# Kernel tuning notes

Measured on AMD Instinct MI355X. Metric: run time of the kernel, lower is better.

## Reference

```python
import jax, jax.numpy as jnp
import numpy as np

D_MODEL = 768
N_HEADS = 12
HEAD_DIM = D_MODEL // N_HEADS
BATCH = 1
SEQ = 4096


def setup_inputs() -> dict:
    key = jax.random.key(0)
    ks = jax.random.split(key, 5)
    std = 1.0 / np.sqrt(D_MODEL)
    return {
        "x": jax.random.normal(ks[0], (BATCH, SEQ, D_MODEL), dtype=jnp.float32),
        "Wq": jax.random.normal(ks[1], (D_MODEL, D_MODEL), dtype=jnp.float32) * std,
        "Wk": jax.random.normal(ks[2], (D_MODEL, D_MODEL), dtype=jnp.float32) * std,
        "Wv": jax.random.normal(ks[3], (D_MODEL, D_MODEL), dtype=jnp.float32) * std,
        "Wp": jax.random.normal(ks[4], (D_MODEL, D_MODEL), dtype=jnp.float32) * std,
    }


def reference(x, Wq, Wk, Wv, Wp):
    B, S, D = x.shape
    scale = HEAD_DIM ** -0.5
    # torch Linear: y = x @ W.T ; reshape to [B, H, S, hd]
    def split_heads(y):
        return y.reshape(B, S, N_HEADS, HEAD_DIM).transpose(0, 2, 1, 3)
    q = split_heads(x @ Wq.T)
    k = split_heads(x @ Wk.T)
    v = split_heads(x @ Wv.T)
    # full [B, H, S, S] scores, as in the original module
    att = jnp.einsum("bhqd,bhkd->bhqk", q, k) * scale
    causal = jnp.tril(jnp.ones((S, S), dtype=bool))
    att = jnp.where(causal[None, None], att, -jnp.inf)
    att = jax.nn.softmax(att, axis=-1)
    y = jnp.einsum("bhqk,bhkd->bhqd", att, v)
    y = y.transpose(0, 2, 1, 3).reshape(B, S, D)
    return y @ Wp.T
```

## Files before the change

kernel.cpp:

```cpp
#include <hip/hip_runtime.h>
#include <hip/hip_bf16.h>
#include <stdint.h>

#define DM 768
#define SQ 4096
#define NH 12

typedef __bf16 bf16;
typedef __bf16 bf16x8 __attribute__((ext_vector_type(8)));
typedef float floatx4 __attribute__((ext_vector_type(4)));
typedef short short4v __attribute__((ext_vector_type(4)));

#if defined(__has_builtin)
#if __has_builtin(__builtin_amdgcn_mfma_f32_16x16x16bf16_1k)
#define HAVE_MFMA16 1
#endif
#endif
#ifndef HAVE_MFMA16
#define HAVE_MFMA16 0
#endif

typedef __attribute__((address_space(1))) const uint32_t cu32_g;
typedef __attribute__((address_space(3))) uint32_t u32_l;

__device__ __forceinline__ uint16_t f2bf(float f) {
  uint32_t u = __builtin_bit_cast(uint32_t, f);
  u += 0x7fff + ((u >> 16) & 1);
  return (uint16_t)(u >> 16);
}

__device__ __forceinline__ uint32_t pk2(float lo, float hi) {
  __hip_bfloat162 h = __float22bfloat162_rn(float2{lo, hi});
  uint32_t u;
  __builtin_memcpy(&u, &h, 4);
  return u;
}

__device__ __forceinline__ float bflo(uint32_t u) {
  return __builtin_bit_cast(float, u << 16);
}
__device__ __forceinline__ float bfhi(uint32_t u) {
  return __builtin_bit_cast(float, u & 0xffff0000u);
}

__device__ __forceinline__ void async16(const bf16* g, bf16* l) {
  __builtin_amdgcn_global_load_lds((cu32_g*)g, (u32_l*)l, 16, 0, 0);
}

__global__ __launch_bounds__(256) void cvt_kernel(
    const float* __restrict__ x, const float* __restrict__ wq,
    const float* __restrict__ wk, const float* __restrict__ wv,
    const float* __restrict__ wp, bf16* __restrict__ xb, bf16* __restrict__ wqb,
    bf16* __restrict__ wkb, bf16* __restrict__ wvb, bf16* __restrict__ wpb) {
  const int XQ = (SQ * DM) / 4;
  const int WQ = (DM * DM) / 4;
  int t = blockIdx.x * 256 + threadIdx.x;
  const float* src;
  bf16* dst;
  int local;
  if (t < XQ) { src = x;  dst = xb;  local = t; }
  else if (t < XQ + WQ)     { src = wq; dst = wqb; local = t - XQ; }
  else if (t < XQ + 2 * WQ) { src = wk; dst = wkb; local = t - XQ - WQ; }
  else if (t < XQ + 3 * WQ) { src = wv; dst = wvb; local = t - XQ - 2 * WQ; }
  else                      { src = wp; dst = wpb; local = t - XQ - 3 * WQ; }
  float4 v = ((const float4*)src)[local];
  ushort4 o;
  o.x = f2bf(v.x); o.y = f2bf(v.y); o.z = f2bf(v.z); o.w = f2bf(v.w);
  ((ushort4*)dst)[local] = o;
}

__device__ __forceinline__ void gemm_core(const bf16* __restrict__ A,
                                          const bf16* __restrict__ B, int m0,
                                          int n0, floatx4 (&acc)[4][4]) {
  __shared__ bf16 lA[2 * 4096];
  __shared__ bf16 lB[2 * 4096];
  const int tid = threadIdx.x;
  const int lane = tid & 63;
  const int w = tid >> 6;

  const int r0 = w * 32 + (lane >> 2);
  const int ke = (((lane & 3) ^ ((lane >> 3) & 3))) * 8;
  const bf16* gA0 = A + (size_t)(m0 + r0) * DM + ke;
  const bf16* gA1 = A + (size_t)(m0 + r0 + 16) * DM + ke;
  const bf16* gB0 = B + (size_t)(n0 + r0) * DM + ke;
  const bf16* gB1 = B + (size_t)(n0 + r0 + 16) * DM + ke;

  async16(gA0, lA + w * 1024); async16(gA1, lA + w * 1024 + 512);
  async16(gB0, lB + w * 1024); async16(gB1, lB + w * 1024 + 512);
  gA0 += 32; gA1 += 32; gB0 += 32; gB1 += 32;

  const int mrow = (w >> 1) * 64 + (lane & 15);
  const int nrow = (w & 1) * 64 + (lane & 15);
  const int cswz = ((lane >> 4) ^ ((lane >> 1) & 3)) * 8;

  for (int kt = 0; kt < DM / 32; ++kt) {
    __syncthreads();
    if (kt + 1 < DM / 32) {
      const int nb = ((kt + 1) & 1) * 4096;
      async16(gA0, lA + nb + w * 1024); async16(gA1, lA + nb + w * 1024 + 512);
      async16(gB0, lB + nb + w * 1024); async16(gB1, lB + nb + w * 1024 + 512);
      gA0 += 32; gA1 += 32; gB0 += 32; gB1 += 32;
    }
    const int cb = (kt & 1) * 4096;
    bf16x8 a[4], b[4];
#pragma unroll
    for (int mt = 0; mt < 4; ++mt)
      a[mt] = *(const bf16x8*)&lA[cb + (mrow + mt * 16) * 32 + cswz];
#pragma unroll
    for (int nt = 0; nt < 4; ++nt)
      b[nt] = *(const bf16x8*)&lB[cb + (nrow + nt * 16) * 32 + cswz];
#pragma unroll
    for (int mt = 0; mt < 4; ++mt)
#pragma unroll
      for (int nt = 0; nt < 4; ++nt)
        acc[mt][nt] = __builtin_amdgcn_mfma_f32_16x16x32_bf16(
            a[mt], b[nt], acc[mt][nt], 0, 0, 0);
  }
}

__global__ __launch_bounds__(256) void qkv_kernel(
    const bf16* __restrict__ xb, const bf16* __restrict__ wq,
    const bf16* __restrict__ wk, const bf16* __restrict__ wv,
    bf16* __restrict__ Qb, bf16* __restrict__ Kb, bf16* __restrict__ Vtb) {
  const int z = blockIdx.z;
  const bf16* B = (z == 0) ? wq : (z == 1) ? wk : wv;
  const int m0 = blockIdx.x * 128, n0 = blockIdx.y * 128;
  floatx4 acc[4][4] = {};
  gemm_core(xb, B, m0, n0, acc);
  const int lane = threadIdx.x & 63, w = threadIdx.x >> 6;
  const int quad = lane >> 4, ql = lane & 15;
  const float qs = (z == 0) ? 0.18033688011112042f : 1.0f;
  if (z < 2) {
    bf16* C = (z == 0) ? Qb : Kb;
#pragma unroll
    for (int mt = 0; mt < 4; ++mt)
#pragma unroll
      for (int nt = 0; nt < 4; ++nt) {
        int row = m0 + (w >> 1) * 64 + mt * 16 + quad * 4;
        int col = n0 + (w & 1) * 64 + nt * 16 + ql;
#pragma unroll
        for (int r = 0; r < 4; ++r)
          *(uint16_t*)&C[(size_t)(row + r) * DM + col] = f2bf(acc[mt][nt][r] * qs);
      }
  } else {
#pragma unroll
    for (int mt = 0; mt < 4; ++mt)
#pragma unroll
      for (int nt = 0; nt < 4; ++nt) {
        int row = m0 + (w >> 1) * 64 + mt * 16 + quad * 4;
        int col = n0 + (w & 1) * 64 + nt * 16 + ql;
        uint32_t lo = pk2(acc[mt][nt][0], acc[mt][nt][1]);
        uint32_t hi = pk2(acc[mt][nt][2], acc[mt][nt][3]);
        *(uint2*)&Vtb[(size_t)col * SQ + row] = make_uint2(lo, hi);
      }
  }
}

__global__ __launch_bounds__(256) void proj_kernel(
    const bf16* __restrict__ Ob, const bf16* __restrict__ wp,
    float* __restrict__ out) {
  __shared__ bf16 lA[2 * 2048];
  __shared__ bf16 lB[2 * 4096];
  const int tid = threadIdx.x, lane = tid & 63, w = tid >> 6;
  const int m0 = blockIdx.x * 64, n0 = blockIdx.y * 128;

  const int ke = (((lane & 3) ^ ((lane >> 3) & 3))) * 8;
  const bf16* gA = Ob + (size_t)(m0 + w * 16 + (lane >> 2)) * DM + ke;
  const bf16* gB0 = wp + (size_t)(n0 + w * 32 + (lane >> 2)) * DM + ke;
  const bf16* gB1 = wp + (size_t)(n0 + w * 32 + (lane >> 2) + 16) * DM + ke;

  async16(gA, lA + w * 512);
  async16(gB0, lB + w * 1024); async16(gB1, lB + w * 1024 + 512);
  gA += 32; gB0 += 32; gB1 += 32;

  const int mrow = (w >> 1) * 32 + (lane & 15);
  const int nrow = (w & 1) * 64 + (lane & 15);
  const int cswz = ((lane >> 4) ^ ((lane >> 1) & 3)) * 8;
  floatx4 acc[2][4] = {};

  for (int kt = 0; kt < DM / 32; ++kt) {
    __syncthreads();
    if (kt + 1 < DM / 32) {
      const int nbA = ((kt + 1) & 1) * 2048, nbB = ((kt + 1) & 1) * 4096;
      async16(gA, lA + nbA + w * 512);
      async16(gB0, lB + nbB + w * 1024); async16(gB1, lB + nbB + w * 1024 + 512);
      gA += 32; gB0 += 32; gB1 += 32;
    }
    const int cbA = (kt & 1) * 2048, cbB = (kt & 1) * 4096;
    bf16x8 a[2], b[4];
#pragma unroll
    for (int mt = 0; mt < 2; ++mt)
      a[mt] = *(const bf16x8*)&lA[cbA + (mrow + mt * 16) * 32 + cswz];
#pragma unroll
    for (int nt = 0; nt < 4; ++nt)
      b[nt] = *(const bf16x8*)&lB[cbB + (nrow + nt * 16) * 32 + cswz];
#pragma unroll
    for (int mt = 0; mt < 2; ++mt)
#pragma unroll
      for (int nt = 0; nt < 4; ++nt)
        acc[mt][nt] = __builtin_amdgcn_mfma_f32_16x16x32_bf16(
            a[mt], b[nt], acc[mt][nt], 0, 0, 0);
  }
  const int quad = lane >> 4, ql = lane & 15;
#pragma unroll
  for (int mt = 0; mt < 2; ++mt)
#pragma unroll
    for (int nt = 0; nt < 4; ++nt) {
      int row = m0 + (w >> 1) * 32 + mt * 16 + quad * 4;
      int col = n0 + (w & 1) * 64 + nt * 16 + ql;
#pragma unroll
      for (int r = 0; r < 4; ++r)
        out[(size_t)(row + r) * DM + col] = acc[mt][nt][r];
    }
}

__global__ __launch_bounds__(256, 4) void attn_kernel(
    const bf16* __restrict__ Qb, const bf16* __restrict__ Kb,
    const bf16* __restrict__ Vtb, uint16_t* __restrict__ OpartB,
    float* __restrict__ Lpart, bf16* __restrict__ Ob) {
#if HAVE_MFMA16
  __shared__ __align__(16) char smem[32768];
#else
  __shared__ __align__(16) char smem[40960];
  bf16* lPt = (bf16*)(smem + 32768);
#endif
  const int tid = threadIdx.x, lane = tid & 63, w = tid >> 6;
  const int quad = lane >> 4, ql = lane & 15;

  int b = blockIdx.x;
  int h = b % NH;
  int i = b / NH;
  int qb, c;
  if (i < 32)      { qb = 31 - (i >> 2); c = i & 3; }
  else if (i < 56) { int t2 = i - 32; qb = 23 - t2 / 3; c = t2 % 3; }
  else if (i < 72) { int t2 = i - 56; qb = 15 - (t2 >> 1); c = t2 & 1; }
  else             { qb = 79 - i; c = 0; }
  const int kv0 = c * 1024;
  const int kv_end = min((qb + 1) * 128, kv0 + 1024);
  const int n_it = (kv_end - kv0) >> 6;
  const bool diag = (kv_end == (qb + 1) * 128);

  bf16x8 qf[2][2];
#pragma unroll
  for (int nt = 0; nt < 2; ++nt)
#pragma unroll
    for (int kt = 0; kt < 2; ++kt)
      qf[nt][kt] = *(const bf16x8*)&Qb[(size_t)(qb * 128 + w * 32 + nt * 16 + ql) * DM +
                                       h * 64 + kt * 32 + quad * 8];

  const int src_e = (((lane & 3) ^ ((lane >> 3) & 3))) * 8;
  const bf16* gK[2];
  const bf16* gV[2];
#pragma unroll
  for (int t = 0; t < 2; ++t) {
    int o = t * 4096 + w * 1024 + lane * 16;
    int cK = o >> 12, rK = (o & 4095) >> 6;
    gK[t] = Kb + (size_t)(kv0 + rK) * DM + h * 64 + cK * 32 + src_e;
    int dV = w * 16 + (lane >> 2);
    gV[t] = Vtb + (size_t)(h * 64 + dV) * SQ + kv0 + t * 32 + src_e;
  }

#pragma unroll
  for (int t = 0; t < 2; ++t) {
    async16(gK[t], (bf16*)(smem + t * 4096 + w * 1024));
    async16(gV[t], (bf16*)(smem + 8192 + t * 4096 + w * 1024));
    gK[t] += 64 * DM;
    gV[t] += 64;
  }

  floatx4 o_acc[4][2] = {};
  float l_s[2] = {0.f, 0.f};
  const int cswz = ((lane >> 4) ^ ((lane >> 1) & 3)) * 8;

  for (int j = 0; j < n_it; ++j) {
    __syncthreads();
    if (j + 1 < n_it) {
      char* dst = smem + ((j + 1) & 1) * 16384;
#pragma unroll
      for (int t = 0; t < 2; ++t) {
        async16(gK[t], (bf16*)(dst + t * 4096 + w * 1024));
        async16(gV[t], (bf16*)(dst + 8192 + t * 4096 + w * 1024));
        gK[t] += 64 * DM;
        gV[t] += 64;
      }
    }
    const char* cbuf = smem + (j & 1) * 16384;
    const bf16* kbuf = (const bf16*)cbuf;
    const char* vbuf = cbuf + 8192;

    floatx4 s[4][2] = {};
#pragma unroll
    for (int kt = 0; kt < 2; ++kt)
#pragma unroll
      for (int mt = 0; mt < 4; ++mt) {
        bf16x8 a = *(const bf16x8*)&kbuf[kt * 2048 + (mt * 16 + ql) * 32 + cswz];
#pragma unroll
        for (int nt = 0; nt < 2; ++nt)
          s[mt][nt] = __builtin_amdgcn_mfma_f32_16x16x32_bf16(a, qf[nt][kt],
                                                              s[mt][nt], 0, 0, 0);
      }

    if (diag && j + 2 >= n_it) {
      const int koff = (j + 1 == n_it) ? 64 : 0;
#pragma unroll
      for (int mt = 0; mt < 4; ++mt)
#pragma unroll
        for (int nt = 0; nt < 2; ++nt)
#pragma unroll
          for (int r = 0; r < 4; ++r) {
            int kpos = koff + mt * 16 + quad * 4 + r;
            int qpos = w * 32 + nt * 16 + ql;
            if (kpos > qpos) s[mt][nt][r] = -1e30f;
          }
    }

    uint2 pp[4][2];
#pragma unroll
    for (int nt = 0; nt < 2; ++nt) {
      float tsum[4];
#pragma unroll
      for (int mt = 0; mt < 4; ++mt) {
        float p0 = __builtin_amdgcn_exp2f(s[mt][nt][0]);
        float p1 = __builtin_amdgcn_exp2f(s[mt][nt][1]);
        float p2 = __builtin_amdgcn_exp2f(s[mt][nt][2]);
        float p3 = __builtin_amdgcn_exp2f(s[mt][nt][3]);
        pp[mt][nt] = make_uint2(pk2(p0, p1), pk2(p2, p3));
        tsum[mt] = (p0 + p1) + (p2 + p3);
      }
      l_s[nt] += (tsum[0] + tsum[1]) + (tsum[2] + tsum[3]);
    }

#if HAVE_MFMA16
#pragma unroll
    for (int mt = 0; mt < 4; ++mt) {
      short4v bfr[2];
#pragma unroll
      for (int nt = 0; nt < 2; ++nt) {
        union { uint2 u; short4v v; } pb;
        pb.u = pp[mt][nt];
        bfr[nt] = pb.v;
      }
      const char* vbase = vbuf + (mt >> 1) * 4096 +
          ((((mt & 1) * 2 + (quad >> 1)) ^ ((ql >> 1) & 3)) * 16) +
          (quad & 1) * 8;
#pragma unroll
      for (int mtd = 0; mtd < 4; ++mtd) {
        short4v a = *(const short4v*)(vbase + (mtd * 16 + ql) * 64);
#pragma unroll
        for (int nt = 0; nt < 2; ++nt)
          o_acc[mtd][nt] = __builtin_amdgcn_mfma_f32_16x16x16bf16_1k(
              a, bfr[nt], o_acc[mtd][nt], 0, 0, 0);
      }
    }
#else
    bf16* lp = lPt + w * 1024;
#pragma unroll
    for (int ks = 0; ks < 2; ++ks) {
#pragma unroll
      for (int nt = 0; nt < 2; ++nt) {
        int q32 = nt * 16 + ql;
        int key = (q32 >> 1) & 7;
#pragma unroll
        for (int mtp = 0; mtp < 2; ++mtp) {
          int slot = mtp * 4 + quad;
          *(uint2*)((char*)lp + q32 * 64 + ((slot ^ key) * 8)) = pp[2 * ks + mtp][nt];
        }
      }
      bf16x8 bp[2];
#pragma unroll
      for (int nt = 0; nt < 2; ++nt) {
        int q32 = nt * 16 + ql;
        int key = (q32 >> 1) & 7;
        union { uint2 u[2]; bf16x8 v; } pb;
        pb.u[0] = *(uint2*)((char*)lp + q32 * 64 + (((2 * quad) ^ key) * 8));
        pb.u[1] = *(uint2*)((char*)lp + q32 * 64 + (((2 * quad + 1) ^ key) * 8));
        bp[nt] = pb.v;
      }
#pragma unroll
      for (int mtd = 0; mtd < 4; ++mtd) {
        bf16x8 a = *(const bf16x8*)((const bf16*)vbuf + ks * 2048 +
                                    (mtd * 16 + ql) * 32 + cswz);
#pragma unroll
        for (int nt = 0; nt < 2; ++nt)
          o_acc[mtd][nt] = __builtin_amdgcn_mfma_f32_16x16x32_bf16(
              a, bp[nt], o_acc[mtd][nt], 0, 0, 0);
      }
    }
#endif
  }

  float lf[2];
#pragma unroll
  for (int nt = 0; nt < 2; ++nt) {
    float ls = l_s[nt];
    ls += __shfl_xor(ls, 16);
    ls += __shfl_xor(ls, 32);
    lf[nt] = ls;
  }

  if (kv0 == 0 && diag) {
#pragma unroll
    for (int nt = 0; nt < 2; ++nt) {
      float rl = 1.0f / lf[nt];
      int qg = qb * 128 + w * 32 + nt * 16 + ql;
#pragma unroll
      for (int mtd = 0; mtd < 4; ++mtd) {
        uint32_t lo = pk2(o_acc[mtd][nt][0] * rl, o_acc[mtd][nt][1] * rl);
        uint32_t hi = pk2(o_acc[mtd][nt][2] * rl, o_acc[mtd][nt][3] * rl);
        *(uint2*)&Ob[(size_t)qg * DM + h * 64 + mtd * 16 + quad * 4] =
            make_uint2(lo, hi);
      }
    }
  } else {
    const int ps = (h * 32 + qb) * 4 + c;
#pragma unroll
    for (int nt = 0; nt < 2; ++nt) {
      int q = w * 32 + nt * 16 + ql;
      if (quad == 0) Lpart[ps * 128 + q] = lf[nt];
#pragma unroll
      for (int mtd = 0; mtd < 4; ++mtd) {
        uint32_t lo = pk2(o_acc[mtd][nt][0], o_acc[mtd][nt][1]);
        uint32_t hi = pk2(o_acc[mtd][nt][2], o_acc[mtd][nt][3]);
        *(uint2*)&OpartB[(size_t)ps * 8192 + q * 64 + mtd * 16 + quad * 4] =
            make_uint2(lo, hi);
      }
    }
  }
}

__global__ __launch_bounds__(256) void combine_kernel(
    const uint16_t* __restrict__ OpartB, const float* __restrict__ Lpart,
    bf16* __restrict__ Ob) {
  int b = blockIdx.x;
  int h = b % NH, qb = 8 + b / NH;
  int nch = (qb + 8) >> 3;
  int t = threadIdx.x;
  int q = t >> 1, dh = (t & 1) * 32;
  int ps0 = (h * 32 + qb) * 4;

  float acc[32] = {};
  float L = 0.f;
#pragma unroll
  for (int cc = 0; cc < 4; ++cc)
    if (cc < nch) {
      L += Lpart[(ps0 + cc) * 128 + q];
      const uint4* p =
          (const uint4*)(OpartB + (size_t)(ps0 + cc) * 8192 + q * 64 + dh);
#pragma unroll
      for (int g = 0; g < 4; ++g) {
        uint4 u = p[g];
        acc[g * 8 + 0] += bflo(u.x); acc[g * 8 + 1] += bfhi(u.x);
        acc[g * 8 + 2] += bflo(u.y); acc[g * 8 + 3] += bfhi(u.y);
        acc[g * 8 + 4] += bflo(u.z); acc[g * 8 + 5] += bfhi(u.z);
        acc[g * 8 + 6] += bflo(u.w); acc[g * 8 + 7] += bfhi(u.w);
      }
    }
  float rl = 1.0f / L;
  bf16* dst = &Ob[(size_t)(qb * 128 + q) * DM + h * 64 + dh];
#pragma unroll
  for (int g = 0; g < 4; ++g) {
    uint4 u;
    u.x = pk2(acc[g * 8 + 0] * rl, acc[g * 8 + 1] * rl);
    u.y = pk2(acc[g * 8 + 2] * rl, acc[g * 8 + 3] * rl);
    u.z = pk2(acc[g * 8 + 4] * rl, acc[g * 8 + 5] * rl);
    u.w = pk2(acc[g * 8 + 6] * rl, acc[g * 8 + 7] * rl);
    *(uint4*)&dst[g * 8] = u;
  }
}

extern "C" void kernel_launch(void* const* d_in, const int* in_sizes, int n_in,
                              void* d_out, int out_size, void* d_ws,
                              size_t ws_size, hipStream_t stream) {
  const float* x  = (const float*)d_in[0];
  const float* wq = (const float*)d_in[1];
  const float* wk = (const float*)d_in[2];
  const float* wv = (const float*)d_in[3];
  const float* wp = (const float*)d_in[4];
  char* ws = (char*)d_ws;
  float* Lpart = (float*)(ws);
  bf16* xb   = (bf16*)(ws);
  bf16* wqb  = (bf16*)(ws + 6291456);
  bf16* wkb  = (bf16*)(ws + 7471104);
  bf16* wvb  = (bf16*)(ws + 8650752);
  bf16* wpb  = (bf16*)(ws + 9830400);
  bf16* Qb   = (bf16*)(ws + 11010048);
  bf16* Kb   = (bf16*)(ws + 17301504);
  bf16* Vtb  = (bf16*)(ws + 23592960);
  bf16* Ob   = (bf16*)(ws + 29884416);
  uint16_t* OpartB = (uint16_t*)(ws + 36175872);

  cvt_kernel<<<5376, 256, 0, stream>>>(x, wq, wk, wv, wp, xb, wqb, wkb, wvb, wpb);
  qkv_kernel<<<dim3(32, 6, 3), 256, 0, stream>>>(xb, wqb, wkb, wvb, Qb, Kb, Vtb);
  attn_kernel<<<960, 256, 0, stream>>>(Qb, Kb, Vtb, OpartB, Lpart, Ob);
  combine_kernel<<<288, 256, 0, stream>>>(OpartB, Lpart, Ob);
  proj_kernel<<<dim3(64, 6), 256, 0, stream>>>(Ob, wpb, (float*)d_out);
}
```

Baseline: 169.8 us.

## Split attention block across 8 waves with 16 query rows each

The attention kernel now launches 512 threads (8 waves) per block, and each wave owns 16 query rows instead of 32. This halves the per-wave accumulator and score register footprint, and each thread issues one async K/V load per tile instead of two. The aim is higher occupancy and better latency hiding. In exchange, each K/V fragment read from shared memory now feeds only one MFMA instead of two, so LDS traffic per FLOP doubles, and the larger block synchronizes more waves per barrier.

```diff
diff --git a/kernel.cpp b/kernel.cpp
--- a/kernel.cpp
+++ b/kernel.cpp
@@ -214,7 +214,7 @@
     }
 }
 
-__global__ __launch_bounds__(256, 4) void attn_kernel(
+__global__ __launch_bounds__(512, 8) void attn_kernel(
     const bf16* __restrict__ Qb, const bf16* __restrict__ Kb,
     const bf16* __restrict__ Vtb, uint16_t* __restrict__ OpartB,
     float* __restrict__ Lpart, bf16* __restrict__ Ob) {
@@ -240,190 +240,140 @@
   const int n_it = (kv_end - kv0) >> 6;
   const bool diag = (kv_end == (qb + 1) * 128);
 
-  bf16x8 qf[2][2];
-#pragma unroll
-  for (int nt = 0; nt < 2; ++nt)
-#pragma unroll
-    for (int kt = 0; kt < 2; ++kt)
-      qf[nt][kt] = *(const bf16x8*)&Qb[(size_t)(qb * 128 + w * 32 + nt * 16 + ql) * DM +
-                                       h * 64 + kt * 32 + quad * 8];
+  bf16x8 qf[2];
+#pragma unroll
+  for (int kt = 0; kt < 2; ++kt)
+    qf[kt] = *(const bf16x8*)&Qb[(size_t)(qb * 128 + w * 16 + ql) * DM +
+                                 h * 64 + kt * 32 + quad * 8];
 
   const int src_e = (((lane & 3) ^ ((lane >> 3) & 3))) * 8;
-  const bf16* gK[2];
-  const bf16* gV[2];
-#pragma unroll
-  for (int t = 0; t < 2; ++t) {
-    int o = t * 4096 + w * 1024 + lane * 16;
-    int cK = o >> 12, rK = (o & 4095) >> 6;
-    gK[t] = Kb + (size_t)(kv0 + rK) * DM + h * 64 + cK * 32 + src_e;
-    int dV = w * 16 + (lane >> 2);
-    gV[t] = Vtb + (size_t)(h * 64 + dV) * SQ + kv0 + t * 32 + src_e;
-  }
-
-#pragma unroll
-  for (int t = 0; t < 2; ++t) {
-    async16(gK[t], (bf16*)(smem + t * 4096 + w * 1024));
-    async16(gV[t], (bf16*)(smem + 8192 + t * 4096 + w * 1024));
-    gK[t] += 64 * DM;
-    gV[t] += 64;
-  }
-
-  floatx4 o_acc[4][2] = {};
-  float l_s[2] = {0.f, 0.f};
+  const int oK = w * 1024 + lane * 16;
+  const int cK = oK >> 12, rK = (oK & 4095) >> 6;
+  const bf16* gK = Kb + (size_t)(kv0 + rK) * DM + h * 64 + cK * 32 + src_e;
+  const int tV = w >> 2;
+  const int dV = (w & 3) * 16 + (lane >> 2);
+  const bf16* gV = Vtb + (size_t)(h * 64 + dV) * SQ + kv0 + tV * 32 + src_e;
+
+  async16(gK, (bf16*)(smem + w * 1024));
+  async16(gV, (bf16*)(smem + 8192 + w * 1024));
+  gK += 64 * DM;
+  gV += 64;
+
+  floatx4 o_acc[4] = {};
+  float l_s = 0.f;
   const int cswz = ((lane >> 4) ^ ((lane >> 1) & 3)) * 8;
 
   for (int j = 0; j < n_it; ++j) {
     __syncthreads();
     if (j + 1 < n_it) {
       char* dst = smem + ((j + 1) & 1) * 16384;
-#pragma unroll
-      for (int t = 0; t < 2; ++t) {
-        async16(gK[t], (bf16*)(dst + t * 4096 + w * 1024));
-        async16(gV[t], (bf16*)(dst + 8192 + t * 4096 + w * 1024));
-        gK[t] += 64 * DM;
-        gV[t] += 64;
-      }
+      async16(gK, (bf16*)(dst + w * 1024));
+      async16(gV, (bf16*)(dst + 8192 + w * 1024));
+      gK += 64 * DM;
+      gV += 64;
     }
     const char* cbuf = smem + (j & 1) * 16384;
     const bf16* kbuf = (const bf16*)cbuf;
     const char* vbuf = cbuf + 8192;
 
-    floatx4 s[4][2] = {};
+    floatx4 s[4] = {};
 #pragma unroll
     for (int kt = 0; kt < 2; ++kt)
 #pragma unroll
       for (int mt = 0; mt < 4; ++mt) {
         bf16x8 a = *(const bf16x8*)&kbuf[kt * 2048 + (mt * 16 + ql) * 32 + cswz];
-#pragma unroll
-        for (int nt = 0; nt < 2; ++nt)
-          s[mt][nt] = __builtin_amdgcn_mfma_f32_16x16x32_bf16(a, qf[nt][kt],
-                                                              s[mt][nt], 0, 0, 0);
+        s[mt] = __builtin_amdgcn_mfma_f32_16x16x32_bf16(a, qf[kt], s[mt], 0, 0, 0);
       }
 
     if (diag && j + 2 >= n_it) {
       const int koff = (j + 1 == n_it) ? 64 : 0;
+      const int qpos = w * 16 + ql;
 #pragma unroll
       for (int mt = 0; mt < 4; ++mt)
 #pragma unroll
-        for (int nt = 0; nt < 2; ++nt)
-#pragma unroll
-          for (int r = 0; r < 4; ++r) {
-            int kpos = koff + mt * 16 + quad * 4 + r;
-            int qpos = w * 32 + nt * 16 + ql;
-            if (kpos > qpos) s[mt][nt][r] = -1e30f;
-          }
-    }
-
-    uint2 pp[4][2];
-#pragma unroll
-    for (int nt = 0; nt < 2; ++nt) {
-      float tsum[4];
-#pragma unroll
-      for (int mt = 0; mt < 4; ++mt) {
-        float p0 = __builtin_amdgcn_exp2f(s[mt][nt][0]);
-        float p1 = __builtin_amdgcn_exp2f(s[mt][nt][1]);
-        float p2 = __builtin_amdgcn_exp2f(s[mt][nt][2]);
-        float p3 = __builtin_amdgcn_exp2f(s[mt][nt][3]);
-        pp[mt][nt] = make_uint2(pk2(p0, p1), pk2(p2, p3));
-        tsum[mt] = (p0 + p1) + (p2 + p3);
-      }
-      l_s[nt] += (tsum[0] + tsum[1]) + (tsum[2] + tsum[3]);
-    }
+        for (int r = 0; r < 4; ++r) {
+          int kpos = koff + mt * 16 + quad * 4 + r;
+          if (kpos > qpos) s[mt][r] = -1e30f;
+        }
+    }
+
+    uint2 pp[4];
+    float tsum[4];
+#pragma unroll
+    for (int mt = 0; mt < 4; ++mt) {
+      float p0 = __builtin_amdgcn_exp2f(s[mt][0]);
+      float p1 = __builtin_amdgcn_exp2f(s[mt][1]);
+      float p2 = __builtin_amdgcn_exp2f(s[mt][2]);
+      float p3 = __builtin_amdgcn_exp2f(s[mt][3]);
+      pp[mt] = make_uint2(pk2(p0, p1), pk2(p2, p3));
+      tsum[mt] = (p0 + p1) + (p2 + p3);
+    }
+    l_s += (tsum[0] + tsum[1]) + (tsum[2] + tsum[3]);
 
 #if HAVE_MFMA16
 #pragma unroll
     for (int mt = 0; mt < 4; ++mt) {
-      short4v bfr[2];
-#pragma unroll
-      for (int nt = 0; nt < 2; ++nt) {
-        union { uint2 u; short4v v; } pb;
-        pb.u = pp[mt][nt];
-        bfr[nt] = pb.v;
-      }
+      union { uint2 u; short4v v; } pb;
+      pb.u = pp[mt];
       const char* vbase = vbuf + (mt >> 1) * 4096 +
           ((((mt & 1) * 2 + (quad >> 1)) ^ ((ql >> 1) & 3)) * 16) +
           (quad & 1) * 8;
 #pragma unroll
       for (int mtd = 0; mtd < 4; ++mtd) {
         short4v a = *(const short4v*)(vbase + (mtd * 16 + ql) * 64);
-#pragma unroll
-        for (int nt = 0; nt < 2; ++nt)
-          o_acc[mtd][nt] = __builtin_amdgcn_mfma_f32_16x16x16bf16_1k(
-              a, bfr[nt], o_acc[mtd][nt], 0, 0, 0);
+        o_acc[mtd] = __builtin_amdgcn_mfma_f32_16x16x16bf16_1k(
+            a, pb.v, o_acc[mtd], 0, 0, 0);
       }
     }
 #else
-    bf16* lp = lPt + w * 1024;
+    bf16* lp = lPt + w * 512;
 #pragma unroll
     for (int ks = 0; ks < 2; ++ks) {
-#pragma unroll
-      for (int nt = 0; nt < 2; ++nt) {
-        int q32 = nt * 16 + ql;
-        int key = (q32 >> 1) & 7;
-#pragma unroll
-        for (int mtp = 0; mtp < 2; ++mtp) {
-          int slot = mtp * 4 + quad;
-          *(uint2*)((char*)lp + q32 * 64 + ((slot ^ key) * 8)) = pp[2 * ks + mtp][nt];
-        }
-      }
-      bf16x8 bp[2];
-#pragma unroll
-      for (int nt = 0; nt < 2; ++nt) {
-        int q32 = nt * 16 + ql;
-        int key = (q32 >> 1) & 7;
-        union { uint2 u[2]; bf16x8 v; } pb;
-        pb.u[0] = *(uint2*)((char*)lp + q32 * 64 + (((2 * quad) ^ key) * 8));
-        pb.u[1] = *(uint2*)((char*)lp + q32 * 64 + (((2 * quad + 1) ^ key) * 8));
-        bp[nt] = pb.v;
-      }
+      int key = (ql >> 1) & 7;
+#pragma unroll
+      for (int mtp = 0; mtp < 2; ++mtp) {
+        int slot = mtp * 4 + quad;
+        *(uint2*)((char*)lp + ql * 64 + ((slot ^ key) * 8)) = pp[2 * ks + mtp];
+      }
+      union { uint2 u[2]; bf16x8 v; } pb;
+      pb.u[0] = *(uint2*)((char*)lp + ql * 64 + (((2 * quad) ^ key) * 8));
+      pb.u[1] = *(uint2*)((char*)lp + ql * 64 + (((2 * quad + 1) ^ key) * 8));
 #pragma unroll
       for (int mtd = 0; mtd < 4; ++mtd) {
         bf16x8 a = *(const bf16x8*)((const bf16*)vbuf + ks * 2048 +
                                     (mtd * 16 + ql) * 32 + cswz);
-#pragma unroll
-        for (int nt = 0; nt < 2; ++nt)
-          o_acc[mtd][nt] = __builtin_amdgcn_mfma_f32_16x16x32_bf16(
-              a, bp[nt], o_acc[mtd][nt], 0, 0, 0);
+        o_acc[mtd] = __builtin_amdgcn_mfma_f32_16x16x32_bf16(
+            a, pb.v, o_acc[mtd], 0, 0, 0);
       }
     }
 #endif
   }
 
-  float lf[2];
-#pragma unroll
-  for (int nt = 0; nt < 2; ++nt) {
-    float ls = l_s[nt];
-    ls += __shfl_xor(ls, 16);
-    ls += __shfl_xor(ls, 32);
-    lf[nt] = ls;
-  }
+  float ls = l_s;
+  ls += __shfl_xor(ls, 16);
+  ls += __shfl_xor(ls, 32);
+  const float lf = ls;
 
   if (kv0 == 0 && diag) {
-#pragma unroll
-    for (int nt = 0; nt < 2; ++nt) {
-      float rl = 1.0f / lf[nt];
-      int qg = qb * 128 + w * 32 + nt * 16 + ql;
-#pragma unroll
-      for (int mtd = 0; mtd < 4; ++mtd) {
-        uint32_t lo = pk2(o_acc[mtd][nt][0] * rl, o_acc[mtd][nt][1] * rl);
-        uint32_t hi = pk2(o_acc[mtd][nt][2] * rl, o_acc[mtd][nt][3] * rl);
-        *(uint2*)&Ob[(size_t)qg * DM + h * 64 + mtd * 16 + quad * 4] =
-            make_uint2(lo, hi);
-      }
+    float rl = 1.0f / lf;
+    int qg = qb * 128 + w * 16 + ql;
+#pragma unroll
+    for (int mtd = 0; mtd < 4; ++mtd) {
+      uint32_t lo = pk2(o_acc[mtd][0] * rl, o_acc[mtd][1] * rl);
+      uint32_t hi = pk2(o_acc[mtd][2] * rl, o_acc[mtd][3] * rl);
+      *(uint2*)&Ob[(size_t)qg * DM + h * 64 + mtd * 16 + quad * 4] =
+          make_uint2(lo, hi);
     }
   } else {
     const int ps = (h * 32 + qb) * 4 + c;
-#pragma unroll
-    for (int nt = 0; nt < 2; ++nt) {
-      int q = w * 32 + nt * 16 + ql;
-      if (quad == 0) Lpart[ps * 128 + q] = lf[nt];
-#pragma unroll
-      for (int mtd = 0; mtd < 4; ++mtd) {
-        uint32_t lo = pk2(o_acc[mtd][nt][0], o_acc[mtd][nt][1]);
-        uint32_t hi = pk2(o_acc[mtd][nt][2], o_acc[mtd][nt][3]);
-        *(uint2*)&OpartB[(size_t)ps * 8192 + q * 64 + mtd * 16 + quad * 4] =
-            make_uint2(lo, hi);
-      }
+    const int q = w * 16 + ql;
+    if (quad == 0) Lpart[ps * 128 + q] = lf;
+#pragma unroll
+    for (int mtd = 0; mtd < 4; ++mtd) {
+      uint32_t lo = pk2(o_acc[mtd][0], o_acc[mtd][1]);
+      uint32_t hi = pk2(o_acc[mtd][2], o_acc[mtd][3]);
+      *(uint2*)&OpartB[(size_t)ps * 8192 + q * 64 + mtd * 16 + quad * 4] =
+          make_uint2(lo, hi);
     }
   }
 }
@@ -491,7 +441,7 @@
 
   cvt_kernel<<<5376, 256, 0, stream>>>(x, wq, wk, wv, wp, xb, wqb, wkb, wvb, wpb);
   qkv_kernel<<<dim3(32, 6, 3), 256, 0, stream>>>(xb, wqb, wkb, wvb, Qb, Kb, Vtb);
-  attn_kernel<<<960, 256, 0, stream>>>(Qb, Kb, Vtb, OpartB, Lpart, Ob);
+  attn_kernel<<<960, 512, 0, stream>>>(Qb, Kb, Vtb, OpartB, Lpart, Ob);
   combine_kernel<<<288, 256, 0, stream>>>(OpartB, Lpart, Ob);
   proj_kernel<<<dim3(64, 6), 256, 0, stream>>>(Ob, wpb, (float*)d_out);
 }
```

Result: slower. 182.3 us (+7.3%).

## Halve attention query tile and split KV across waves with LDS reduction

Applied to the files above, without the earlier changes.

The attention kernel now processes 64-query tiles instead of 128. Each workgroup's four waves are split into two query halves by two KV halves, and the two KV-half partial outputs and row sums are reduced through shared memory at the end. A constexpr table orders (query block, chunk) work items by descending length for load balancing, and the grid doubles to 1920 blocks, with the combine kernel adapted to match. The aim is more parallelism and better tail balance, at the cost of an extra LDS reduction, reloading K/V per smaller tile, and more partial-result traffic.

```diff
diff --git a/kernel.cpp b/kernel.cpp
--- a/kernel.cpp
+++ b/kernel.cpp
@@ -46,6 +46,25 @@
 __device__ __forceinline__ void async16(const bf16* g, bf16* l) {
   __builtin_amdgcn_global_load_lds((cu32_g*)g, (u32_l*)l, 16, 0, 0);
 }
+
+struct MapT { uint16_t v[160]; };
+static constexpr MapT make_map() {
+  MapT m{};
+  int idx = 0;
+  for (int nit = 16; nit >= 1; --nit)
+    for (int qb = 63; qb >= 0; --qb) {
+      int len = (qb + 1) * 64;
+      int nch = (len + 1023) >> 10;
+      for (int c = nch - 1; c >= 0; --c) {
+        int cs = c * 1024;
+        int ce = (len < cs + 1024) ? len : cs + 1024;
+        int ni = (ce - cs) >> 6;
+        if (ni == nit) m.v[idx++] = (uint16_t)(qb * 4 + c);
+      }
+    }
+  return m;
+}
+__device__ __constant__ MapT kMap = make_map();
 
 __global__ __launch_bounds__(256) void cvt_kernel(
     const float* __restrict__ x, const float* __restrict__ wq,
@@ -214,7 +233,7 @@
     }
 }
 
-__global__ __launch_bounds__(256, 4) void attn_kernel(
+__global__ __launch_bounds__(256, 5) void attn_kernel(
     const bf16* __restrict__ Qb, const bf16* __restrict__ Kb,
     const bf16* __restrict__ Vtb, uint16_t* __restrict__ OpartB,
     float* __restrict__ Lpart, bf16* __restrict__ Ob) {
@@ -226,26 +245,26 @@
 #endif
   const int tid = threadIdx.x, lane = tid & 63, w = tid >> 6;
   const int quad = lane >> 4, ql = lane & 15;
+  const int qh = w & 1;
+  const int kh = w >> 1;
 
   int b = blockIdx.x;
   int h = b % NH;
   int i = b / NH;
-  int qb, c;
-  if (i < 32)      { qb = 31 - (i >> 2); c = i & 3; }
-  else if (i < 56) { int t2 = i - 32; qb = 23 - t2 / 3; c = t2 % 3; }
-  else if (i < 72) { int t2 = i - 56; qb = 15 - (t2 >> 1); c = t2 & 1; }
-  else             { qb = 79 - i; c = 0; }
+  int e = kMap.v[i];
+  int qb = e >> 2, c = e & 3;
   const int kv0 = c * 1024;
-  const int kv_end = min((qb + 1) * 128, kv0 + 1024);
+  const int qlen = (qb + 1) * 64;
+  const int kv_end = min(qlen, kv0 + 1024);
   const int n_it = (kv_end - kv0) >> 6;
-  const bool diag = (kv_end == (qb + 1) * 128);
+  const bool diag = (kv_end == qlen);
 
   bf16x8 qf[2][2];
 #pragma unroll
   for (int nt = 0; nt < 2; ++nt)
 #pragma unroll
     for (int kt = 0; kt < 2; ++kt)
-      qf[nt][kt] = *(const bf16x8*)&Qb[(size_t)(qb * 128 + w * 32 + nt * 16 + ql) * DM +
+      qf[nt][kt] = *(const bf16x8*)&Qb[(size_t)(qb * 64 + qh * 32 + nt * 16 + ql) * DM +
                                        h * 64 + kt * 32 + quad * 8];
 
   const int src_e = (((lane & 3) ^ ((lane >> 3) & 3))) * 8;
@@ -288,38 +307,38 @@
     const bf16* kbuf = (const bf16*)cbuf;
     const char* vbuf = cbuf + 8192;
 
-    floatx4 s[4][2] = {};
+    floatx4 s[2][2] = {};
 #pragma unroll
     for (int kt = 0; kt < 2; ++kt)
 #pragma unroll
-      for (int mt = 0; mt < 4; ++mt) {
-        bf16x8 a = *(const bf16x8*)&kbuf[kt * 2048 + (mt * 16 + ql) * 32 + cswz];
+      for (int mt = 0; mt < 2; ++mt) {
+        bf16x8 a = *(const bf16x8*)&kbuf[kt * 2048 + (kh * 32 + mt * 16 + ql) * 32 + cswz];
 #pragma unroll
         for (int nt = 0; nt < 2; ++nt)
           s[mt][nt] = __builtin_amdgcn_mfma_f32_16x16x32_bf16(a, qf[nt][kt],
                                                               s[mt][nt], 0, 0, 0);
       }
 
-    if (diag && j + 2 >= n_it) {
-      const int koff = (j + 1 == n_it) ? 64 : 0;
-#pragma unroll
-      for (int mt = 0; mt < 4; ++mt)
-#pragma unroll
-        for (int nt = 0; nt < 2; ++nt)
+    if (diag && j == n_it - 1) {
+#pragma unroll
+      for (int mt = 0; mt < 2; ++mt)
+#pragma unroll
+        for (int nt = 0; nt < 2; ++nt) {
+          const int qpos = qh * 32 + nt * 16 + ql;
 #pragma unroll
           for (int r = 0; r < 4; ++r) {
-            int kpos = koff + mt * 16 + quad * 4 + r;
-            int qpos = w * 32 + nt * 16 + ql;
+            int kpos = kh * 32 + mt * 16 + quad * 4 + r;
             if (kpos > qpos) s[mt][nt][r] = -1e30f;
           }
-    }
-
-    uint2 pp[4][2];
+        }
+    }
+
+    uint2 pp[2][2];
 #pragma unroll
     for (int nt = 0; nt < 2; ++nt) {
-      float tsum[4];
-#pragma unroll
-      for (int mt = 0; mt < 4; ++mt) {
+      float tsum[2];
+#pragma unroll
+      for (int mt = 0; mt < 2; ++mt) {
         float p0 = __builtin_amdgcn_exp2f(s[mt][nt][0]);
         float p1 = __builtin_amdgcn_exp2f(s[mt][nt][1]);
         float p2 = __builtin_amdgcn_exp2f(s[mt][nt][2]);
@@ -327,12 +346,12 @@
         pp[mt][nt] = make_uint2(pk2(p0, p1), pk2(p2, p3));
         tsum[mt] = (p0 + p1) + (p2 + p3);
       }
-      l_s[nt] += (tsum[0] + tsum[1]) + (tsum[2] + tsum[3]);
+      l_s[nt] += tsum[0] + tsum[1];
     }
 
 #if HAVE_MFMA16
 #pragma unroll
-    for (int mt = 0; mt < 4; ++mt) {
+    for (int mt = 0; mt < 2; ++mt) {
       short4v bfr[2];
 #pragma unroll
       for (int nt = 0; nt < 2; ++nt) {
@@ -340,8 +359,8 @@
         pb.u = pp[mt][nt];
         bfr[nt] = pb.v;
       }
-      const char* vbase = vbuf + (mt >> 1) * 4096 +
-          ((((mt & 1) * 2 + (quad >> 1)) ^ ((ql >> 1) & 3)) * 16) +
+      const char* vbase = vbuf + kh * 4096 +
+          (((mt * 2 + (quad >> 1)) ^ ((ql >> 1) & 3)) * 16) +
           (quad & 1) * 8;
 #pragma unroll
       for (int mtd = 0; mtd < 4; ++mtd) {
@@ -354,8 +373,7 @@
     }
 #else
     bf16* lp = lPt + w * 1024;
-#pragma unroll
-    for (int ks = 0; ks < 2; ++ks) {
+    {
 #pragma unroll
       for (int nt = 0; nt < 2; ++nt) {
         int q32 = nt * 16 + ql;
@@ -363,7 +381,7 @@
 #pragma unroll
         for (int mtp = 0; mtp < 2; ++mtp) {
           int slot = mtp * 4 + quad;
-          *(uint2*)((char*)lp + q32 * 64 + ((slot ^ key) * 8)) = pp[2 * ks + mtp][nt];
+          *(uint2*)((char*)lp + q32 * 64 + ((slot ^ key) * 8)) = pp[mtp][nt];
         }
       }
       bf16x8 bp[2];
@@ -378,7 +396,7 @@
       }
 #pragma unroll
       for (int mtd = 0; mtd < 4; ++mtd) {
-        bf16x8 a = *(const bf16x8*)((const bf16*)vbuf + ks * 2048 +
+        bf16x8 a = *(const bf16x8*)((const bf16*)vbuf + kh * 2048 +
                                     (mtd * 16 + ql) * 32 + cswz);
 #pragma unroll
         for (int nt = 0; nt < 2; ++nt)
@@ -389,40 +407,66 @@
 #endif
   }
 
-  float lf[2];
-#pragma unroll
-  for (int nt = 0; nt < 2; ++nt) {
-    float ls = l_s[nt];
-    ls += __shfl_xor(ls, 16);
-    ls += __shfl_xor(ls, 32);
-    lf[nt] = ls;
-  }
-
-  if (kv0 == 0 && diag) {
+  char* fb = smem + ((n_it & 1) * 16384);
+  char* lb = smem + (((n_it - 1) & 1) * 16384);
+  __syncthreads();
+  if (kh == 1) {
+    char* po = fb + (w - 2) * 8192;
+#pragma unroll
+    for (int nt = 0; nt < 2; ++nt)
+#pragma unroll
+      for (int mtd = 0; mtd < 4; ++mtd)
+        *(floatx4*)(po + (nt * 4 + mtd) * 1024 + lane * 16) = o_acc[mtd][nt];
+    float2* pl = (float2*)(lb + (w - 2) * 512);
+    pl[lane] = make_float2(l_s[0], l_s[1]);
+  }
+  __syncthreads();
+  if (kh == 0) {
+    char* po = fb + w * 8192;
+#pragma unroll
+    for (int nt = 0; nt < 2; ++nt)
+#pragma unroll
+      for (int mtd = 0; mtd < 4; ++mtd)
+        o_acc[mtd][nt] += *(const floatx4*)(po + (nt * 4 + mtd) * 1024 + lane * 16);
+    float2 l2 = ((const float2*)(lb + w * 512))[lane];
+    l_s[0] += l2.x;
+    l_s[1] += l2.y;
+
+    float lf[2];
 #pragma unroll
     for (int nt = 0; nt < 2; ++nt) {
-      float rl = 1.0f / lf[nt];
-      int qg = qb * 128 + w * 32 + nt * 16 + ql;
-#pragma unroll
-      for (int mtd = 0; mtd < 4; ++mtd) {
-        uint32_t lo = pk2(o_acc[mtd][nt][0] * rl, o_acc[mtd][nt][1] * rl);
-        uint32_t hi = pk2(o_acc[mtd][nt][2] * rl, o_acc[mtd][nt][3] * rl);
-        *(uint2*)&Ob[(size_t)qg * DM + h * 64 + mtd * 16 + quad * 4] =
-            make_uint2(lo, hi);
-      }
-    }
-  } else {
-    const int ps = (h * 32 + qb) * 4 + c;
-#pragma unroll
-    for (int nt = 0; nt < 2; ++nt) {
-      int q = w * 32 + nt * 16 + ql;
-      if (quad == 0) Lpart[ps * 128 + q] = lf[nt];
-#pragma unroll
-      for (int mtd = 0; mtd < 4; ++mtd) {
-        uint32_t lo = pk2(o_acc[mtd][nt][0], o_acc[mtd][nt][1]);
-        uint32_t hi = pk2(o_acc[mtd][nt][2], o_acc[mtd][nt][3]);
-        *(uint2*)&OpartB[(size_t)ps * 8192 + q * 64 + mtd * 16 + quad * 4] =
-            make_uint2(lo, hi);
+      float ls = l_s[nt];
+      ls += __shfl_xor(ls, 16);
+      ls += __shfl_xor(ls, 32);
+      lf[nt] = ls;
+    }
+
+    if (qb < 16) {
+#pragma unroll
+      for (int nt = 0; nt < 2; ++nt) {
+        float rl = 1.0f / lf[nt];
+        int qg = qb * 64 + qh * 32 + nt * 16 + ql;
+#pragma unroll
+        for (int mtd = 0; mtd < 4; ++mtd) {
+          uint32_t lo = pk2(o_acc[mtd][nt][0] * rl, o_acc[mtd][nt][1] * rl);
+          uint32_t hi = pk2(o_acc[mtd][nt][2] * rl, o_acc[mtd][nt][3] * rl);
+          *(uint2*)&Ob[(size_t)qg * DM + h * 64 + mtd * 16 + quad * 4] =
+              make_uint2(lo, hi);
+        }
+      }
+    } else {
+      const int ps = (h * 64 + qb) * 4 + c;
+#pragma unroll
+      for (int nt = 0; nt < 2; ++nt) {
+        int q = qh * 32 + nt * 16 + ql;
+        if (quad == 0) Lpart[ps * 64 + q] = lf[nt];
+#pragma unroll
+        for (int mtd = 0; mtd < 4; ++mtd) {
+          uint32_t lo = pk2(o_acc[mtd][nt][0], o_acc[mtd][nt][1]);
+          uint32_t hi = pk2(o_acc[mtd][nt][2], o_acc[mtd][nt][3]);
+          *(uint2*)&OpartB[(size_t)ps * 4096 + q * 64 + mtd * 16 + quad * 4] =
+              make_uint2(lo, hi);
+        }
       }
     }
   }
@@ -432,22 +476,22 @@
     const uint16_t* __restrict__ OpartB, const float* __restrict__ Lpart,
     bf16* __restrict__ Ob) {
   int b = blockIdx.x;
-  int h = b % NH, qb = 8 + b / NH;
-  int nch = (qb + 8) >> 3;
+  int h = b % NH, qb = 16 + b / NH;
+  int nch = (qb + 16) >> 4;
   int t = threadIdx.x;
-  int q = t >> 1, dh = (t & 1) * 32;
-  int ps0 = (h * 32 + qb) * 4;
-
-  float acc[32] = {};
+  int q = t >> 2, dh = (t & 3) * 16;
+  int ps0 = (h * 64 + qb) * 4;
+
+  float acc[16] = {};
   float L = 0.f;
 #pragma unroll
   for (int cc = 0; cc < 4; ++cc)
     if (cc < nch) {
-      L += Lpart[(ps0 + cc) * 128 + q];
+      L += Lpart[(ps0 + cc) * 64 + q];
       const uint4* p =
-          (const uint4*)(OpartB + (size_t)(ps0 + cc) * 8192 + q * 64 + dh);
-#pragma unroll
-      for (int g = 0; g < 4; ++g) {
+          (const uint4*)(OpartB + (size_t)(ps0 + cc) * 4096 + q * 64 + dh);
+#pragma unroll
+      for (int g = 0; g < 2; ++g) {
         uint4 u = p[g];
         acc[g * 8 + 0] += bflo(u.x); acc[g * 8 + 1] += bfhi(u.x);
         acc[g * 8 + 2] += bflo(u.y); acc[g * 8 + 3] += bfhi(u.y);
@@ -456,9 +500,9 @@
       }
     }
   float rl = 1.0f / L;
-  bf16* dst = &Ob[(size_t)(qb * 128 + q) * DM + h * 64 + dh];
-#pragma unroll
-  for (int g = 0; g < 4; ++g) {
+  bf16* dst = &Ob[(size_t)(qb * 64 + q) * DM + h * 64 + dh];
+#pragma unroll
+  for (int g = 0; g < 2; ++g) {
     uint4 u;
     u.x = pk2(acc[g * 8 + 0] * rl, acc[g * 8 + 1] * rl);
     u.y = pk2(acc[g * 8 + 2] * rl, acc[g * 8 + 3] * rl);
@@ -491,7 +535,7 @@
 
   cvt_kernel<<<5376, 256, 0, stream>>>(x, wq, wk, wv, wp, xb, wqb, wkb, wvb, wpb);
   qkv_kernel<<<dim3(32, 6, 3), 256, 0, stream>>>(xb, wqb, wkb, wvb, Qb, Kb, Vtb);
-  attn_kernel<<<960, 256, 0, stream>>>(Qb, Kb, Vtb, OpartB, Lpart, Ob);
-  combine_kernel<<<288, 256, 0, stream>>>(OpartB, Lpart, Ob);
+  attn_kernel<<<1920, 256, 0, stream>>>(Qb, Kb, Vtb, OpartB, Lpart, Ob);
+  combine_kernel<<<576, 256, 0, stream>>>(OpartB, Lpart, Ob);
   proj_kernel<<<dim3(64, 6), 256, 0, stream>>>(Ob, wpb, (float*)d_out);
 }
```

Result: faster. 162.9 us (-4.1%).

## Split attention KV tile across wave pairs with 512-thread blocks and LDS reduction

Applied to the files above, without the earlier changes.

The attention kernel now launches 8 waves per block instead of 4. Each pair of waves shares a 32-row query slice and splits the 64-key tile between them, so every wave does half the QK and PV work per iteration. K/V loads are spread over twice as many threads. The two partial output accumulators and row sums are reduced through shared memory at the end. This trades extra synchronisation and an LDS reduction for more waves in flight and lower per-wave register pressure, which aims to improve latency hiding in the attention loop.

```diff
diff --git a/kernel.cpp b/kernel.cpp
--- a/kernel.cpp
+++ b/kernel.cpp
@@ -214,18 +214,20 @@
     }
 }
 
-__global__ __launch_bounds__(256, 4) void attn_kernel(
+__global__ __launch_bounds__(512, 8) void attn_kernel(
     const bf16* __restrict__ Qb, const bf16* __restrict__ Kb,
     const bf16* __restrict__ Vtb, uint16_t* __restrict__ OpartB,
     float* __restrict__ Lpart, bf16* __restrict__ Ob) {
 #if HAVE_MFMA16
   __shared__ __align__(16) char smem[32768];
 #else
-  __shared__ __align__(16) char smem[40960];
+  __shared__ __align__(16) char smem[49152];
   bf16* lPt = (bf16*)(smem + 32768);
 #endif
   const int tid = threadIdx.x, lane = tid & 63, w = tid >> 6;
   const int quad = lane >> 4, ql = lane & 15;
+  const int qh = w >> 1;
+  const int kh = w & 1;
 
   int b = blockIdx.x;
   int h = b % NH;
@@ -245,28 +247,21 @@
   for (int nt = 0; nt < 2; ++nt)
 #pragma unroll
     for (int kt = 0; kt < 2; ++kt)
-      qf[nt][kt] = *(const bf16x8*)&Qb[(size_t)(qb * 128 + w * 32 + nt * 16 + ql) * DM +
+      qf[nt][kt] = *(const bf16x8*)&Qb[(size_t)(qb * 128 + qh * 32 + nt * 16 + ql) * DM +
                                        h * 64 + kt * 32 + quad * 8];
 
   const int src_e = (((lane & 3) ^ ((lane >> 3) & 3))) * 8;
-  const bf16* gK[2];
-  const bf16* gV[2];
-#pragma unroll
-  for (int t = 0; t < 2; ++t) {
-    int o = t * 4096 + w * 1024 + lane * 16;
-    int cK = o >> 12, rK = (o & 4095) >> 6;
-    gK[t] = Kb + (size_t)(kv0 + rK) * DM + h * 64 + cK * 32 + src_e;
-    int dV = w * 16 + (lane >> 2);
-    gV[t] = Vtb + (size_t)(h * 64 + dV) * SQ + kv0 + t * 32 + src_e;
-  }
-
-#pragma unroll
-  for (int t = 0; t < 2; ++t) {
-    async16(gK[t], (bf16*)(smem + t * 4096 + w * 1024));
-    async16(gV[t], (bf16*)(smem + 8192 + t * 4096 + w * 1024));
-    gK[t] += 64 * DM;
-    gV[t] += 64;
-  }
+  const int oK = w * 1024 + lane * 16;
+  const int cK = oK >> 12, rK = (oK & 4095) >> 6;
+  const bf16* gK = Kb + (size_t)(kv0 + rK) * DM + h * 64 + cK * 32 + src_e;
+  const int tV = w >> 2;
+  const int dV = (w & 3) * 16 + (lane >> 2);
+  const bf16* gV = Vtb + (size_t)(h * 64 + dV) * SQ + kv0 + tV * 32 + src_e;
+
+  async16(gK, (bf16*)(smem + w * 1024));
+  async16(gV, (bf16*)(smem + 8192 + w * 1024));
+  gK += 64 * DM;
+  gV += 64;
 
   floatx4 o_acc[4][2] = {};
   float l_s[2] = {0.f, 0.f};
@@ -276,24 +271,21 @@
     __syncthreads();
     if (j + 1 < n_it) {
       char* dst = smem + ((j + 1) & 1) * 16384;
-#pragma unroll
-      for (int t = 0; t < 2; ++t) {
-        async16(gK[t], (bf16*)(dst + t * 4096 + w * 1024));
-        async16(gV[t], (bf16*)(dst + 8192 + t * 4096 + w * 1024));
-        gK[t] += 64 * DM;
-        gV[t] += 64;
-      }
+      async16(gK, (bf16*)(dst + w * 1024));
+      async16(gV, (bf16*)(dst + 8192 + w * 1024));
+      gK += 64 * DM;
+      gV += 64;
     }
     const char* cbuf = smem + (j & 1) * 16384;
     const bf16* kbuf = (const bf16*)cbuf;
     const char* vbuf = cbuf + 8192;
 
-    floatx4 s[4][2] = {};
+    floatx4 s[2][2] = {};
 #pragma unroll
     for (int kt = 0; kt < 2; ++kt)
 #pragma unroll
-      for (int mt = 0; mt < 4; ++mt) {
-        bf16x8 a = *(const bf16x8*)&kbuf[kt * 2048 + (mt * 16 + ql) * 32 + cswz];
+      for (int mt = 0; mt < 2; ++mt) {
+        bf16x8 a = *(const bf16x8*)&kbuf[kt * 2048 + (kh * 32 + mt * 16 + ql) * 32 + cswz];
 #pragma unroll
         for (int nt = 0; nt < 2; ++nt)
           s[mt][nt] = __builtin_amdgcn_mfma_f32_16x16x32_bf16(a, qf[nt][kt],
@@ -303,23 +295,24 @@
     if (diag && j + 2 >= n_it) {
       const int koff = (j + 1 == n_it) ? 64 : 0;
 #pragma unroll
-      for (int mt = 0; mt < 4; ++mt)
-#pragma unroll
-        for (int nt = 0; nt < 2; ++nt)
+      for (int mt = 0; mt < 2; ++mt)
+#pragma unroll
+        for (int nt = 0; nt < 2; ++nt) {
+          const int qpos = qh * 32 + nt * 16 + ql;
 #pragma unroll
           for (int r = 0; r < 4; ++r) {
-            int kpos = koff + mt * 16 + quad * 4 + r;
-            int qpos = w * 32 + nt * 16 + ql;
+            int kpos = koff + kh * 32 + mt * 16 + quad * 4 + r;
             if (kpos > qpos) s[mt][nt][r] = -1e30f;
           }
-    }
-
-    uint2 pp[4][2];
+        }
+    }
+
+    uint2 pp[2][2];
 #pragma unroll
     for (int nt = 0; nt < 2; ++nt) {
-      float tsum[4];
-#pragma unroll
-      for (int mt = 0; mt < 4; ++mt) {
+      float tsum[2];
+#pragma unroll
+      for (int mt = 0; mt < 2; ++mt) {
         float p0 = __builtin_amdgcn_exp2f(s[mt][nt][0]);
         float p1 = __builtin_amdgcn_exp2f(s[mt][nt][1]);
         float p2 = __builtin_amdgcn_exp2f(s[mt][nt][2]);
@@ -327,12 +320,12 @@
         pp[mt][nt] = make_uint2(pk2(p0, p1), pk2(p2, p3));
         tsum[mt] = (p0 + p1) + (p2 + p3);
       }
-      l_s[nt] += (tsum[0] + tsum[1]) + (tsum[2] + tsum[3]);
+      l_s[nt] += tsum[0] + tsum[1];
     }
 
 #if HAVE_MFMA16
 #pragma unroll
-    for (int mt = 0; mt < 4; ++mt) {
+    for (int mt = 0; mt < 2; ++mt) {
       short4v bfr[2];
 #pragma unroll
       for (int nt = 0; nt < 2; ++nt) {
@@ -340,8 +333,8 @@
         pb.u = pp[mt][nt];
         bfr[nt] = pb.v;
       }
-      const char* vbase = vbuf + (mt >> 1) * 4096 +
-          ((((mt & 1) * 2 + (quad >> 1)) ^ ((ql >> 1) & 3)) * 16) +
+      const char* vbase = vbuf + kh * 4096 +
+          (((mt * 2 + (quad >> 1)) ^ ((ql >> 1) & 3)) * 16) +
           (quad & 1) * 8;
 #pragma unroll
       for (int mtd = 0; mtd < 4; ++mtd) {
@@ -354,8 +347,7 @@
     }
 #else
     bf16* lp = lPt + w * 1024;
-#pragma unroll
-    for (int ks = 0; ks < 2; ++ks) {
+    {
 #pragma unroll
       for (int nt = 0; nt < 2; ++nt) {
         int q32 = nt * 16 + ql;
@@ -363,7 +355,7 @@
 #pragma unroll
         for (int mtp = 0; mtp < 2; ++mtp) {
           int slot = mtp * 4 + quad;
-          *(uint2*)((char*)lp + q32 * 64 + ((slot ^ key) * 8)) = pp[2 * ks + mtp][nt];
+          *(uint2*)((char*)lp + q32 * 64 + ((slot ^ key) * 8)) = pp[mtp][nt];
         }
       }
       bf16x8 bp[2];
@@ -378,7 +370,7 @@
       }
 #pragma unroll
       for (int mtd = 0; mtd < 4; ++mtd) {
-        bf16x8 a = *(const bf16x8*)((const bf16*)vbuf + ks * 2048 +
+        bf16x8 a = *(const bf16x8*)((const bf16*)vbuf + kh * 2048 +
                                     (mtd * 16 + ql) * 32 + cswz);
 #pragma unroll
         for (int nt = 0; nt < 2; ++nt)
@@ -389,40 +381,68 @@
 #endif
   }
 
-  float lf[2];
-#pragma unroll
-  for (int nt = 0; nt < 2; ++nt) {
-    float ls = l_s[nt];
-    ls += __shfl_xor(ls, 16);
-    ls += __shfl_xor(ls, 32);
-    lf[nt] = ls;
-  }
-
-  if (kv0 == 0 && diag) {
+  __syncthreads();
+  if (kh == 1) {
+    char* po = smem + qh * 8192;
+#pragma unroll
+    for (int nt = 0; nt < 2; ++nt)
+#pragma unroll
+      for (int mtd = 0; mtd < 4; ++mtd)
+        *(floatx4*)(po + (nt * 4 + mtd) * 1024 + lane * 16) = o_acc[mtd][nt];
+  }
+  __syncthreads();
+  if (kh == 0) {
+    char* po = smem + qh * 8192;
+#pragma unroll
+    for (int nt = 0; nt < 2; ++nt)
+#pragma unroll
+      for (int mtd = 0; mtd < 4; ++mtd)
+        o_acc[mtd][nt] += *(const floatx4*)(po + (nt * 4 + mtd) * 1024 + lane * 16);
+  }
+  __syncthreads();
+  if (kh == 1)
+    *(float2*)(smem + qh * 512 + lane * 8) = make_float2(l_s[0], l_s[1]);
+  __syncthreads();
+  if (kh == 0) {
+    float2 l2 = *(const float2*)(smem + qh * 512 + lane * 8);
+    l_s[0] += l2.x;
+    l_s[1] += l2.y;
+
+    float lf[2];
 #pragma unroll
     for (int nt = 0; nt < 2; ++nt) {
-      float rl = 1.0f / lf[nt];
-      int qg = qb * 128 + w * 32 + nt * 16 + ql;
-#pragma unroll
-      for (int mtd = 0; mtd < 4; ++mtd) {
-        uint32_t lo = pk2(o_acc[mtd][nt][0] * rl, o_acc[mtd][nt][1] * rl);
-        uint32_t hi = pk2(o_acc[mtd][nt][2] * rl, o_acc[mtd][nt][3] * rl);
-        *(uint2*)&Ob[(size_t)qg * DM + h * 64 + mtd * 16 + quad * 4] =
-            make_uint2(lo, hi);
-      }
-    }
-  } else {
-    const int ps = (h * 32 + qb) * 4 + c;
-#pragma unroll
-    for (int nt = 0; nt < 2; ++nt) {
-      int q = w * 32 + nt * 16 + ql;
-      if (quad == 0) Lpart[ps * 128 + q] = lf[nt];
-#pragma unroll
-      for (int mtd = 0; mtd < 4; ++mtd) {
-        uint32_t lo = pk2(o_acc[mtd][nt][0], o_acc[mtd][nt][1]);
-        uint32_t hi = pk2(o_acc[mtd][nt][2], o_acc[mtd][nt][3]);
-        *(uint2*)&OpartB[(size_t)ps * 8192 + q * 64 + mtd * 16 + quad * 4] =
-            make_uint2(lo, hi);
+      float ls = l_s[nt];
+      ls += __shfl_xor(ls, 16);
+      ls += __shfl_xor(ls, 32);
+      lf[nt] = ls;
+    }
+
+    if (kv0 == 0 && diag) {
+#pragma unroll
+      for (int nt = 0; nt < 2; ++nt) {
+        float rl = 1.0f / lf[nt];
+        int qg = qb * 128 + qh * 32 + nt * 16 + ql;
+#pragma unroll
+        for (int mtd = 0; mtd < 4; ++mtd) {
+          uint32_t lo = pk2(o_acc[mtd][nt][0] * rl, o_acc[mtd][nt][1] * rl);
+          uint32_t hi = pk2(o_acc[mtd][nt][2] * rl, o_acc[mtd][nt][3] * rl);
+          *(uint2*)&Ob[(size_t)qg * DM + h * 64 + mtd * 16 + quad * 4] =
+              make_uint2(lo, hi);
+        }
+      }
+    } else {
+      const int ps = (h * 32 + qb) * 4 + c;
+#pragma unroll
+      for (int nt = 0; nt < 2; ++nt) {
+        int q = qh * 32 + nt * 16 + ql;
+        if (quad == 0) Lpart[ps * 128 + q] = lf[nt];
+#pragma unroll
+        for (int mtd = 0; mtd < 4; ++mtd) {
+          uint32_t lo = pk2(o_acc[mtd][nt][0], o_acc[mtd][nt][1]);
+          uint32_t hi = pk2(o_acc[mtd][nt][2], o_acc[mtd][nt][3]);
+          *(uint2*)&OpartB[(size_t)ps * 8192 + q * 64 + mtd * 16 + quad * 4] =
+              make_uint2(lo, hi);
+        }
       }
     }
   }
@@ -491,7 +511,7 @@
 
   cvt_kernel<<<5376, 256, 0, stream>>>(x, wq, wk, wv, wp, xb, wqb, wkb, wvb, wpb);
   qkv_kernel<<<dim3(32, 6, 3), 256, 0, stream>>>(xb, wqb, wkb, wvb, Qb, Kb, Vtb);
-  attn_kernel<<<960, 256, 0, stream>>>(Qb, Kb, Vtb, OpartB, Lpart, Ob);
+  attn_kernel<<<960, 512, 0, stream>>>(Qb, Kb, Vtb, OpartB, Lpart, Ob);
   combine_kernel<<<288, 256, 0, stream>>>(OpartB, Lpart, Ob);
   proj_kernel<<<dim3(64, 6), 256, 0, stream>>>(Ob, wpb, (float*)d_out);
 }
```

New measurement: 338.6 us. 99.4% more time.
